# Kernel optimization log

Measured on AMD Instinct MI355X. Metric: run time of the kernel, lower is better.

Reference implementation:

```python
import jax, jax.numpy as jnp
import numpy as np

N = 50000
E = 800000
IN_F = 128
HID = 64
HEADS = 4
OUT_F = 2
NEG_SLOPE = 0.2


def setup_inputs() -> dict:
    key = jax.random.key(0)
    ks = jax.random.split(key, 16)
    feat = jax.random.normal(ks[0], (N, IN_F), dtype=jnp.float32)
    src = jax.random.randint(ks[1], (E,), 0, N, dtype=jnp.int32)
    dst = jax.random.randint(ks[2], (E,), 0, N, dtype=jnp.int32)
    s1 = 1.0 / np.sqrt(IN_F)
    s2 = 1.0 / np.sqrt(HID * HEADS)
    W1s = jax.random.uniform(ks[3], (IN_F, HEADS * HID), jnp.float32, -s1, s1)
    b1s = jnp.zeros((HEADS * HID,), jnp.float32)
    W1d = jax.random.uniform(ks[4], (IN_F, HEADS * HID), jnp.float32, -s1, s1)
    b1d = jnp.zeros((HEADS * HID,), jnp.float32)
    attn1 = jax.random.uniform(ks[5], (HEADS, HID), jnp.float32, -s1, s1)
    W2s = jax.random.uniform(ks[6], (HEADS * HID, OUT_F), jnp.float32, -s2, s2)
    b2s = jnp.zeros((OUT_F,), jnp.float32)
    W2d = jax.random.uniform(ks[7], (HEADS * HID, OUT_F), jnp.float32, -s2, s2)
    b2d = jnp.zeros((OUT_F,), jnp.float32)
    attn2 = jax.random.uniform(ks[8], (1, OUT_F), jnp.float32, -s2, s2)
    return {"feat": feat, "src": src, "dst": dst,
            "W1s": W1s, "b1s": b1s, "W1d": W1d, "b1d": b1d, "attn1": attn1,
            "W2s": W2s, "b2s": b2s, "W2d": W2d, "b2d": b2d, "attn2": attn2}


def gatv2_layer(x, src, dst, Ws, bs, Wd, bd, attn):
    # x: [N, F_in]; attn: [H, D]
    H, D = attn.shape
    hs = (x @ Ws + bs).reshape(-1, H, D)  # [N, H, D] source projection
    hd = (x @ Wd + bd).reshape(-1, H, D)  # [N, H, D] dest projection
    e = jax.nn.leaky_relu(hs[src] + hd[dst], NEG_SLOPE)        # [E, H, D]
    score = jnp.einsum('ehd,hd->eh', e, attn)                  # [E, H]
    # segment softmax over incoming edges of each dst node
    m = jax.ops.segment_max(score, dst, num_segments=N)        # [N, H]
    m = jnp.where(jnp.isfinite(m), m, 0.0)
    ex = jnp.exp(score - m[dst])                               # [E, H]
    denom = jax.ops.segment_sum(ex, dst, num_segments=N)       # [N, H]
    alpha = ex / jnp.where(denom[dst] > 0, denom[dst], 1.0)    # [E, H]
    out = jax.ops.segment_sum(alpha[:, :, None] * hs[src], dst, num_segments=N)
    return out  # [N, H, D]


def reference(feat, src, dst, W1s, b1s, W1d, b1d, attn1, W2s, b2s, W2d, b2d, attn2):
    h = gatv2_layer(feat, src, dst, W1s, b1s, W1d, b1d, attn1)  # [N, 4, 64]
    h = jax.nn.elu(h).reshape(h.shape[0], -1)                    # [N, 256]
    h = gatv2_layer(h, src, dst, W2s, b2s, W2d, b2d, attn2)      # [N, 1, 2]
    return h[:, 0, :]                                            # [N, 2]
```

## Files before the change

### kernel.cpp

```cpp
#include <hip/hip_runtime.h>
#include <math.h>

#define NN 50000
#define NE 800000
#define NEG 0.2f
#define NB 196

typedef __attribute__((ext_vector_type(8))) short bf16x8;
typedef __attribute__((ext_vector_type(4))) float f32x4;
typedef __attribute__((ext_vector_type(4))) _Float16 half4;

__device__ __forceinline__ unsigned short bf16_rne(float x)
{
    unsigned u = __float_as_uint(x);
    return (unsigned short)((u + 0x7FFF + ((u >> 16) & 1)) >> 16);
}
__device__ __forceinline__ float bf16_to_f(unsigned short h)
{
    return __uint_as_float(((unsigned)h) << 16);
}

__global__ __launch_bounds__(256) void cvt_feat(
    const float* __restrict__ f, unsigned short* __restrict__ hi,
    unsigned short* __restrict__ lo)
{
    const int i = blockIdx.x * 256 + threadIdx.x;
    if (i >= NN * 128 / 4) return;
    const float4 v = reinterpret_cast<const float4*>(f)[i];
    ushort4 h, l;
    h.x = bf16_rne(v.x); l.x = bf16_rne(v.x - bf16_to_f(h.x));
    h.y = bf16_rne(v.y); l.y = bf16_rne(v.y - bf16_to_f(h.y));
    h.z = bf16_rne(v.z); l.z = bf16_rne(v.z - bf16_to_f(h.z));
    h.w = bf16_rne(v.w); l.w = bf16_rne(v.w - bf16_to_f(h.w));
    reinterpret_cast<ushort4*>(hi)[i] = h;
    reinterpret_cast<ushort4*>(lo)[i] = l;
}

__global__ __launch_bounds__(256) void cvt_w(
    const float* __restrict__ Ws, const float* __restrict__ Wd,
    unsigned short* __restrict__ ShiP, unsigned short* __restrict__ SloP,
    unsigned short* __restrict__ DhiP, unsigned short* __restrict__ DloP)
{
    const int idx = blockIdx.x * 256 + threadIdx.x;
    const float* W = blockIdx.y ? Wd : Ws;
    unsigned short* oh = blockIdx.y ? DhiP : ShiP;
    unsigned short* ol = blockIdx.y ? DloP : SloP;
    const int j  = idx & 7;
    const int l  = (idx >> 3) & 63;
    const int ct = (idx >> 9) & 15;
    const int ks = idx >> 13;
    const int k   = ks * 32 + ((l >> 4) << 3) + j;
    const int col = (ct << 4) + (l & 15);
    const float x = W[(size_t)k * 256 + col];
    const unsigned short h = bf16_rne(x);
    oh[idx] = h;
    ol[idx] = bf16_rne(x - bf16_to_f(h));
}

__global__ __launch_bounds__(256) void gemm_mfma(
    const unsigned short* __restrict__ fhi, const unsigned short* __restrict__ flo,
    const unsigned short* __restrict__ WhS, const unsigned short* __restrict__ WlS,
    const float* __restrict__ bS, _Float16* __restrict__ outS,
    const unsigned short* __restrict__ WhD, const unsigned short* __restrict__ WlD,
    const float* __restrict__ bD, float* __restrict__ outD)
{
    const unsigned short* Wh = blockIdx.y ? WhD : WhS;
    const unsigned short* Wl = blockIdx.y ? WlD : WlS;
    const float* bv = blockIdx.y ? bD : bS;

    const int tid = threadIdx.x;
    const int w   = tid >> 6;
    const int l   = tid & 63;
    const int r16 = l & 15;
    const int kg  = l >> 4;
    const int row0 = blockIdx.x * 64;

    int arow = row0 + w * 16 + r16;
    if (arow >= NN) arow = NN - 1;

    f32x4 acc[16];
#pragma unroll
    for (int ct = 0; ct < 16; ++ct) acc[ct] = (f32x4){0.f, 0.f, 0.f, 0.f};

#pragma unroll
    for (int ks = 0; ks < 4; ++ks) {
        const bf16x8 ah = *reinterpret_cast<const bf16x8*>(
            &fhi[(size_t)arow * 128 + ks * 32 + kg * 8]);
        const bf16x8 al = *reinterpret_cast<const bf16x8*>(
            &flo[(size_t)arow * 128 + ks * 32 + kg * 8]);
#pragma unroll
        for (int ct = 0; ct < 16; ++ct) {
            const size_t boff = ((size_t)(ks * 16 + ct) * 64 + l) * 8;
            const bf16x8 bh = *reinterpret_cast<const bf16x8*>(&Wh[boff]);
            const bf16x8 bl = *reinterpret_cast<const bf16x8*>(&Wl[boff]);
            acc[ct] = __builtin_amdgcn_mfma_f32_16x16x32_bf16(ah, bh, acc[ct], 0, 0, 0);
            acc[ct] = __builtin_amdgcn_mfma_f32_16x16x32_bf16(ah, bl, acc[ct], 0, 0, 0);
            acc[ct] = __builtin_amdgcn_mfma_f32_16x16x32_bf16(al, bh, acc[ct], 0, 0, 0);
        }
    }

    const int orow0 = row0 + w * 16 + kg * 4;
    if (blockIdx.y == 0) {
#pragma unroll
        for (int ct = 0; ct < 16; ++ct) {
            const int col = ct * 16 + r16;
            const float bias = bv[col];
#pragma unroll
            for (int reg = 0; reg < 4; ++reg) {
                const int orow = orow0 + reg;
                if (orow < NN)
                    outS[(size_t)orow * 256 + col] = (_Float16)(acc[ct][reg] + bias);
            }
        }
    } else {
#pragma unroll
        for (int ct = 0; ct < 16; ++ct) {
            const int col = ct * 16 + r16;
            const float bias = bv[col];
#pragma unroll
            for (int reg = 0; reg < 4; ++reg) {
                const int orow = orow0 + reg;
                if (orow < NN)
                    outD[(size_t)orow * 256 + col] = acc[ct][reg] + bias;
            }
        }
    }
}

__global__ void count_deg(const int* __restrict__ dst, int* __restrict__ deg)
{
    int e = blockIdx.x * blockDim.x + threadIdx.x;
    if (e < NE) atomicAdd(&deg[dst[e]], 1);
}

__global__ __launch_bounds__(256) void deg_blocksum(const int* __restrict__ deg,
                                                    int* __restrict__ bsum)
{
    int i = blockIdx.x * 256 + threadIdx.x;
    int v = (i < NN) ? deg[i] : 0;
#pragma unroll
    for (int off = 32; off; off >>= 1) v += __shfl_xor(v, off);
    __shared__ int ws[4];
    if ((threadIdx.x & 63) == 0) ws[threadIdx.x >> 6] = v;
    __syncthreads();
    if (threadIdx.x == 0) bsum[blockIdx.x] = ws[0] + ws[1] + ws[2] + ws[3];
}

__global__ __launch_bounds__(256) void scan_bsum(int* __restrict__ bsum)
{
    __shared__ int tmp[256];
    int t = threadIdx.x;
    int orig = (t < NB) ? bsum[t] : 0;
    tmp[t] = orig;
    __syncthreads();
    for (int off = 1; off < 256; off <<= 1) {
        int v = (t >= off) ? tmp[t - off] : 0;
        __syncthreads();
        tmp[t] += v;
        __syncthreads();
    }
    if (t < NB) bsum[t] = tmp[t] - orig;
}

__global__ __launch_bounds__(256) void write_rows(const int* __restrict__ deg,
                                                  const int* __restrict__ bpre,
                                                  int* __restrict__ row_start,
                                                  int* __restrict__ cursor)
{
    int i = blockIdx.x * 256 + threadIdx.x;
    int d = (i < NN) ? deg[i] : 0;
    int lane = threadIdx.x & 63, w = threadIdx.x >> 6;
    int x = d;
#pragma unroll
    for (int off = 1; off < 64; off <<= 1) {
        int v = __shfl_up(x, off);
        if (lane >= off) x += v;
    }
    __shared__ int wsum[4];
    if (lane == 63) wsum[w] = x;
    __syncthreads();
    int woff = 0;
#pragma unroll
    for (int k = 0; k < 4; ++k)
        if (k < w) woff += wsum[k];
    if (i < NN) {
        int rs = bpre[blockIdx.x] + woff + x - d;
        row_start[i] = rs;
        cursor[i] = rs;
    }
    if (blockIdx.x == 0 && threadIdx.x == 0) row_start[NN] = NE;
}

__global__ void scatter_src(const int* __restrict__ src, const int* __restrict__ dst,
                            int* __restrict__ cursor, int* __restrict__ src_sorted)
{
    int e = blockIdx.x * blockDim.x + threadIdx.x;
    if (e < NE) {
        int pos = atomicAdd(&cursor[dst[e]], 1);
        src_sorted[pos] = src[e];
    }
}

__global__ __launch_bounds__(256) void gat1_fused(
    const _Float16* __restrict__ hs, const float* __restrict__ hd,
    const float* __restrict__ attn, const int* __restrict__ src_sorted,
    const int* __restrict__ row_start,
    const float* __restrict__ W2s, const float* __restrict__ b2s,
    const float* __restrict__ W2d, const float* __restrict__ b2d,
    float* __restrict__ hs2, float* __restrict__ hd2)
{
    const int n = blockIdx.x * 4 + (threadIdx.x >> 6);
    const int lane = threadIdx.x & 63;
    const int beg = row_start[n], end_ = row_start[n + 1];

    const float4 a4 = *reinterpret_cast<const float4*>(&attn[lane * 4]);
    const float4 y4 = *reinterpret_cast<const float4*>(&hd[(size_t)n * 256 + lane * 4]);

    float m = -INFINITY, den = 0.0f;
    float4 acc = make_float4(0.f, 0.f, 0.f, 0.f);

#define SCORE(xf, p)                                                        \
    {                                                                       \
        float t;                                                            \
        t = xf.x + y4.x; t = fmaxf(t, NEG * t); p = t * a4.x;               \
        t = xf.y + y4.y; t = fmaxf(t, NEG * t); p = fmaf(t, a4.y, p);       \
        t = xf.z + y4.z; t = fmaxf(t, NEG * t); p = fmaf(t, a4.z, p);       \
        t = xf.w + y4.w; t = fmaxf(t, NEG * t); p = fmaf(t, a4.w, p);       \
    }
#define UPDATE(xf, p)                                                       \
    {                                                                       \
        if (p > m + 8.0f) {                                                 \
            const float rs = __expf(m - p);                                 \
            den *= rs;                                                      \
            acc.x *= rs; acc.y *= rs; acc.z *= rs; acc.w *= rs;             \
            m = p;                                                          \
        }                                                                   \
        const float wv = __expf(p - m);                                     \
        den += wv;                                                          \
        acc.x = fmaf(wv, xf.x, acc.x);                                      \
        acc.y = fmaf(wv, xf.y, acc.y);                                      \
        acc.z = fmaf(wv, xf.z, acc.z);                                      \
        acc.w = fmaf(wv, xf.w, acc.w);                                      \
    }

    int i = beg;
    for (; i + 3 < end_; i += 4) {
        const int s0 = __builtin_amdgcn_readfirstlane(src_sorted[i]);
        const int s1 = __builtin_amdgcn_readfirstlane(src_sorted[i + 1]);
        const int s2 = __builtin_amdgcn_readfirstlane(src_sorted[i + 2]);
        const int s3 = __builtin_amdgcn_readfirstlane(src_sorted[i + 3]);
        const half4 h0 = *reinterpret_cast<const half4*>(&hs[(size_t)s0 * 256 + lane * 4]);
        const half4 h1 = *reinterpret_cast<const half4*>(&hs[(size_t)s1 * 256 + lane * 4]);
        const half4 h2 = *reinterpret_cast<const half4*>(&hs[(size_t)s2 * 256 + lane * 4]);
        const half4 h3 = *reinterpret_cast<const half4*>(&hs[(size_t)s3 * 256 + lane * 4]);
        const float4 x0 = make_float4(h0.x, h0.y, h0.z, h0.w);
        const float4 x1 = make_float4(h1.x, h1.y, h1.z, h1.w);
        const float4 x2 = make_float4(h2.x, h2.y, h2.z, h2.w);
        const float4 x3 = make_float4(h3.x, h3.y, h3.z, h3.w);
        float p0, p1, p2, p3;
        SCORE(x0, p0) SCORE(x1, p1) SCORE(x2, p2) SCORE(x3, p3)
        p0 += __shfl_xor(p0, 1); p1 += __shfl_xor(p1, 1);
        p2 += __shfl_xor(p2, 1); p3 += __shfl_xor(p3, 1);
        p0 += __shfl_xor(p0, 2); p1 += __shfl_xor(p1, 2);
        p2 += __shfl_xor(p2, 2); p3 += __shfl_xor(p3, 2);
        p0 += __shfl_xor(p0, 4); p1 += __shfl_xor(p1, 4);
        p2 += __shfl_xor(p2, 4); p3 += __shfl_xor(p3, 4);
        p0 += __shfl_xor(p0, 8); p1 += __shfl_xor(p1, 8);
        p2 += __shfl_xor(p2, 8); p3 += __shfl_xor(p3, 8);
        UPDATE(x0, p0) UPDATE(x1, p1) UPDATE(x2, p2) UPDATE(x3, p3)
    }
    for (; i < end_; ++i) {
        const int s = __builtin_amdgcn_readfirstlane(src_sorted[i]);
        const half4 hx = *reinterpret_cast<const half4*>(&hs[(size_t)s * 256 + lane * 4]);
        const float4 x = make_float4(hx.x, hx.y, hx.z, hx.w);
        float p;
        SCORE(x, p)
        p += __shfl_xor(p, 1);
        p += __shfl_xor(p, 2);
        p += __shfl_xor(p, 4);
        p += __shfl_xor(p, 8);
        UPDATE(x, p)
    }
#undef SCORE
#undef UPDATE

    const float inv = (den > 0.0f) ? 1.0f / den : 0.0f;
    float4 o;
    o.x = acc.x * inv; o.y = acc.y * inv; o.z = acc.z * inv; o.w = acc.w * inv;
    o.x = (o.x > 0.0f) ? o.x : __expf(o.x) - 1.0f;
    o.y = (o.y > 0.0f) ? o.y : __expf(o.y) - 1.0f;
    o.z = (o.z > 0.0f) ? o.z : __expf(o.z) - 1.0f;
    o.w = (o.w > 0.0f) ? o.w : __expf(o.w) - 1.0f;

    const float4 wsa = *reinterpret_cast<const float4*>(&W2s[lane * 8]);
    const float4 wsb = *reinterpret_cast<const float4*>(&W2s[lane * 8 + 4]);
    const float4 wda = *reinterpret_cast<const float4*>(&W2d[lane * 8]);
    const float4 wdb = *reinterpret_cast<const float4*>(&W2d[lane * 8 + 4]);
    float ps0 = o.x * wsa.x + o.y * wsa.z + o.z * wsb.x + o.w * wsb.z;
    float ps1 = o.x * wsa.y + o.y * wsa.w + o.z * wsb.y + o.w * wsb.w;
    float pd0 = o.x * wda.x + o.y * wda.z + o.z * wdb.x + o.w * wdb.z;
    float pd1 = o.x * wda.y + o.y * wda.w + o.z * wdb.y + o.w * wdb.w;
#pragma unroll
    for (int off = 32; off; off >>= 1) {
        ps0 += __shfl_xor(ps0, off);
        ps1 += __shfl_xor(ps1, off);
        pd0 += __shfl_xor(pd0, off);
        pd1 += __shfl_xor(pd1, off);
    }
    if (lane == 0) {
        hs2[(size_t)n * 2 + 0] = ps0 + b2s[0];
        hs2[(size_t)n * 2 + 1] = ps1 + b2s[1];
        hd2[(size_t)n * 2 + 0] = pd0 + b2d[0];
        hd2[(size_t)n * 2 + 1] = pd1 + b2d[1];
    }
}

__global__ __launch_bounds__(256) void node2_kernel(
    const float* __restrict__ hs2, const float* __restrict__ hd2,
    const float* __restrict__ attn2, const int* __restrict__ src_sorted,
    const int* __restrict__ row_start, float* __restrict__ out)
{
    const int n = blockIdx.x * 16 + (threadIdx.x >> 4);
    const int q = threadIdx.x & 15;
    if (n >= NN) return;
    const float a0 = attn2[0], a1 = attn2[1];
    const float h0 = hd2[n * 2 + 0], h1v = hd2[n * 2 + 1];
    const int beg = row_start[n], end_ = row_start[n + 1];
    float m = -INFINITY, den = 0.0f, A0 = 0.0f, A1 = 0.0f;
    for (int i = beg + q; i < end_; i += 16) {
        const int s = src_sorted[i];
        float x0 = hs2[s * 2 + 0], x1 = hs2[s * 2 + 1];
        float t0 = x0 + h0;  t0 = fmaxf(t0, NEG * t0);
        float t1 = x1 + h1v; t1 = fmaxf(t1, NEG * t1);
        float p = fmaf(t0, a0, t1 * a1);
        float mn = fmaxf(m, p);
        float c = __expf(m - mn);
        float w = __expf(p - mn);
        den = den * c + w;
        A0 = A0 * c + w * x0;
        A1 = A1 * c + w * x1;
        m = mn;
    }
#pragma unroll
    for (int off = 1; off < 16; off <<= 1) {
        float m2 = __shfl_xor(m, off, 16);
        float d2 = __shfl_xor(den, off, 16);
        float b0 = __shfl_xor(A0, off, 16);
        float b1 = __shfl_xor(A1, off, 16);
        float mn = fmaxf(m, m2);
        float c1 = (m < mn) ? __expf(m - mn) : 1.0f;
        float c2 = (m2 < mn) ? __expf(m2 - mn) : 1.0f;
        den = den * c1 + d2 * c2;
        A0 = A0 * c1 + b0 * c2;
        A1 = A1 * c1 + b1 * c2;
        m = mn;
    }
    if (q == 0) {
        out[n * 2 + 0] = (den > 0.0f) ? A0 / den : 0.0f;
        out[n * 2 + 1] = (den > 0.0f) ? A1 / den : 0.0f;
    }
}

extern "C" void kernel_launch(void* const* d_in, const int* in_sizes, int n_in,
                              void* d_out, int out_size, void* d_ws, size_t ws_size,
                              hipStream_t stream)
{
    const float* feat  = (const float*)d_in[0];
    const int*   src   = (const int*)d_in[1];
    const int*   dst   = (const int*)d_in[2];
    const float* W1s   = (const float*)d_in[3];
    const float* b1s   = (const float*)d_in[4];
    const float* W1d   = (const float*)d_in[5];
    const float* b1d   = (const float*)d_in[6];
    const float* attn1 = (const float*)d_in[7];
    const float* W2s   = (const float*)d_in[8];
    const float* b2s   = (const float*)d_in[9];
    const float* W2d   = (const float*)d_in[10];
    const float* b2d   = (const float*)d_in[11];
    const float* attn2 = (const float*)d_in[12];
    float* out = (float*)d_out;

    char* ws = (char*)d_ws;
    size_t off = 0;
    auto alloc = [&](size_t bytes) {
        char* p = ws + off;
        off += (bytes + 255) & ~size_t(255);
        return p;
    };
    _Float16*       hs1h       = (_Float16*)alloc((size_t)NN * 256 * 2);
    float*          hd1        = (float*)alloc((size_t)NN * 256 * 4);
    unsigned short* fb_hi      = (unsigned short*)alloc((size_t)NN * 128 * 2);
    unsigned short* fb_lo      = (unsigned short*)alloc((size_t)NN * 128 * 2);
    unsigned short* wbs_hi     = (unsigned short*)alloc((size_t)128 * 256 * 2);
    unsigned short* wbs_lo     = (unsigned short*)alloc((size_t)128 * 256 * 2);
    unsigned short* wbd_hi     = (unsigned short*)alloc((size_t)128 * 256 * 2);
    unsigned short* wbd_lo     = (unsigned short*)alloc((size_t)128 * 256 * 2);
    int*            src_sorted = (int*)alloc((size_t)NE * 4);
    int*            row_start  = (int*)alloc((size_t)(NN + 1) * 4);
    int*            deg        = (int*)alloc((size_t)NN * 4);
    int*            cursor     = (int*)alloc((size_t)NN * 4);
    int*            bsum       = (int*)alloc((size_t)NB * 4);
    float*          hs2        = (float*)alloc((size_t)NN * 2 * 4);
    float*          hd2        = (float*)alloc((size_t)NN * 2 * 4);
    (void)ws_size; (void)n_in; (void)in_sizes; (void)out_size;

    hipMemsetAsync(deg, 0, (size_t)NN * 4, stream);

    cvt_feat<<<(NN * 128 / 4 + 255) / 256, 256, 0, stream>>>(feat, fb_hi, fb_lo);
    dim3 wgrid(128, 2);
    cvt_w<<<wgrid, 256, 0, stream>>>(W1s, W1d, wbs_hi, wbs_lo, wbd_hi, wbd_lo);
    dim3 ggrid((NN + 63) / 64, 2);
    gemm_mfma<<<ggrid, 256, 0, stream>>>(fb_hi, fb_lo,
                                         wbs_hi, wbs_lo, b1s, hs1h,
                                         wbd_hi, wbd_lo, b1d, hd1);

    const int eb = (NE + 255) / 256;
    count_deg<<<eb, 256, 0, stream>>>(dst, deg);
    deg_blocksum<<<NB, 256, 0, stream>>>(deg, bsum);
    scan_bsum<<<1, 256, 0, stream>>>(bsum);
    write_rows<<<NB, 256, 0, stream>>>(deg, bsum, row_start, cursor);
    scatter_src<<<eb, 256, 0, stream>>>(src, dst, cursor, src_sorted);

    gat1_fused<<<NN / 4, 256, 0, stream>>>(hs1h, hd1, attn1, src_sorted, row_start,
                                           W2s, b2s, W2d, b2d, hs2, hd2);

    node2_kernel<<<(NN + 15) / 16, 256, 0, stream>>>(hs2, hd2, attn2, src_sorted,
                                                     row_start, out);
}
```

Before: 269.5 us.

## Fuse feature bf16 split into GEMM and halve-wave edge processing with fp16 dot

Removes the separate cvt_feat kernel and its hi/lo buffers by splitting fp32 features into bf16 hi/lo inside the GEMM's A-operand load. Rewrites the layer-1 aggregation so each half-wave handles a different edge, with 8 fp16 elements per lane. The leaky-relu score is computed in packed fp16 with fdot2, and the two halves' online-softmax states are merged at the end. This cuts global traffic and the instruction count per edge, at the cost of reduced score precision from fp16 arithmetic and duplicated feature conversion across the two GEMM y-blocks.

```diff
diff --git a/kernel.cpp b/kernel.cpp
--- a/kernel.cpp
+++ b/kernel.cpp
@@ -8,7 +8,10 @@
 
 typedef __attribute__((ext_vector_type(8))) short bf16x8;
 typedef __attribute__((ext_vector_type(4))) float f32x4;
-typedef __attribute__((ext_vector_type(4))) _Float16 half4;
+typedef __attribute__((ext_vector_type(8))) _Float16 half8;
+typedef __attribute__((ext_vector_type(2))) _Float16 half2v;
+
+#define PAIR(v, k) (__builtin_shufflevector(v, v, 2 * (k), 2 * (k) + 1))
 
 __device__ __forceinline__ unsigned short bf16_rne(float x)
 {
@@ -18,22 +21,6 @@
 __device__ __forceinline__ float bf16_to_f(unsigned short h)
 {
     return __uint_as_float(((unsigned)h) << 16);
-}
-
-__global__ __launch_bounds__(256) void cvt_feat(
-    const float* __restrict__ f, unsigned short* __restrict__ hi,
-    unsigned short* __restrict__ lo)
-{
-    const int i = blockIdx.x * 256 + threadIdx.x;
-    if (i >= NN * 128 / 4) return;
-    const float4 v = reinterpret_cast<const float4*>(f)[i];
-    ushort4 h, l;
-    h.x = bf16_rne(v.x); l.x = bf16_rne(v.x - bf16_to_f(h.x));
-    h.y = bf16_rne(v.y); l.y = bf16_rne(v.y - bf16_to_f(h.y));
-    h.z = bf16_rne(v.z); l.z = bf16_rne(v.z - bf16_to_f(h.z));
-    h.w = bf16_rne(v.w); l.w = bf16_rne(v.w - bf16_to_f(h.w));
-    reinterpret_cast<ushort4*>(hi)[i] = h;
-    reinterpret_cast<ushort4*>(lo)[i] = l;
 }
 
 __global__ __launch_bounds__(256) void cvt_w(
@@ -58,7 +45,7 @@
 }
 
 __global__ __launch_bounds__(256) void gemm_mfma(
-    const unsigned short* __restrict__ fhi, const unsigned short* __restrict__ flo,
+    const float* __restrict__ feat,
     const unsigned short* __restrict__ WhS, const unsigned short* __restrict__ WlS,
     const float* __restrict__ bS, _Float16* __restrict__ outS,
     const unsigned short* __restrict__ WhD, const unsigned short* __restrict__ WlD,
@@ -84,10 +71,18 @@
 
 #pragma unroll
     for (int ks = 0; ks < 4; ++ks) {
-        const bf16x8 ah = *reinterpret_cast<const bf16x8*>(
-            &fhi[(size_t)arow * 128 + ks * 32 + kg * 8]);
-        const bf16x8 al = *reinterpret_cast<const bf16x8*>(
-            &flo[(size_t)arow * 128 + ks * 32 + kg * 8]);
+        const float4 fa = *reinterpret_cast<const float4*>(
+            &feat[(size_t)arow * 128 + ks * 32 + kg * 8]);
+        const float4 fb = *reinterpret_cast<const float4*>(
+            &feat[(size_t)arow * 128 + ks * 32 + kg * 8 + 4]);
+        const float fv[8] = {fa.x, fa.y, fa.z, fa.w, fb.x, fb.y, fb.z, fb.w};
+        bf16x8 ah, al;
+#pragma unroll
+        for (int j = 0; j < 8; ++j) {
+            const unsigned short h = bf16_rne(fv[j]);
+            ah[j] = (short)h;
+            al[j] = (short)bf16_rne(fv[j] - bf16_to_f(h));
+        }
 #pragma unroll
         for (int ct = 0; ct < 16; ++ct) {
             const size_t boff = ((size_t)(ks * 16 + ct) * 64 + l) * 8;
@@ -211,107 +206,140 @@
 {
     const int n = blockIdx.x * 4 + (threadIdx.x >> 6);
     const int lane = threadIdx.x & 63;
+    const int half_id = lane >> 5;
+    const int sl = lane & 31;
     const int beg = row_start[n], end_ = row_start[n + 1];
 
-    const float4 a4 = *reinterpret_cast<const float4*>(&attn[lane * 4]);
-    const float4 y4 = *reinterpret_cast<const float4*>(&hd[(size_t)n * 256 + lane * 4]);
+    const float4 af0 = *reinterpret_cast<const float4*>(&attn[sl * 8 + 0]);
+    const float4 af1 = *reinterpret_cast<const float4*>(&attn[sl * 8 + 4]);
+    const float4 yf0 = *reinterpret_cast<const float4*>(&hd[(size_t)n * 256 + sl * 8 + 0]);
+    const float4 yf1 = *reinterpret_cast<const float4*>(&hd[(size_t)n * 256 + sl * 8 + 4]);
+    half8 ah, yh;
+    ah[0] = (_Float16)af0.x; ah[1] = (_Float16)af0.y; ah[2] = (_Float16)af0.z; ah[3] = (_Float16)af0.w;
+    ah[4] = (_Float16)af1.x; ah[5] = (_Float16)af1.y; ah[6] = (_Float16)af1.z; ah[7] = (_Float16)af1.w;
+    yh[0] = (_Float16)yf0.x; yh[1] = (_Float16)yf0.y; yh[2] = (_Float16)yf0.z; yh[3] = (_Float16)yf0.w;
+    yh[4] = (_Float16)yf1.x; yh[5] = (_Float16)yf1.y; yh[6] = (_Float16)yf1.z; yh[7] = (_Float16)yf1.w;
+    const _Float16 NEGH = (_Float16)NEG;
 
     float m = -INFINITY, den = 0.0f;
-    float4 acc = make_float4(0.f, 0.f, 0.f, 0.f);
-
-#define SCORE(xf, p)                                                        \
-    {                                                                       \
-        float t;                                                            \
-        t = xf.x + y4.x; t = fmaxf(t, NEG * t); p = t * a4.x;               \
-        t = xf.y + y4.y; t = fmaxf(t, NEG * t); p = fmaf(t, a4.y, p);       \
-        t = xf.z + y4.z; t = fmaxf(t, NEG * t); p = fmaf(t, a4.z, p);       \
-        t = xf.w + y4.w; t = fmaxf(t, NEG * t); p = fmaf(t, a4.w, p);       \
-    }
-#define UPDATE(xf, p)                                                       \
-    {                                                                       \
-        if (p > m + 8.0f) {                                                 \
-            const float rs = __expf(m - p);                                 \
-            den *= rs;                                                      \
-            acc.x *= rs; acc.y *= rs; acc.z *= rs; acc.w *= rs;             \
-            m = p;                                                          \
-        }                                                                   \
-        const float wv = __expf(p - m);                                     \
-        den += wv;                                                          \
-        acc.x = fmaf(wv, xf.x, acc.x);                                      \
-        acc.y = fmaf(wv, xf.y, acc.y);                                      \
-        acc.z = fmaf(wv, xf.z, acc.z);                                      \
-        acc.w = fmaf(wv, xf.w, acc.w);                                      \
-    }
-
-    int i = beg;
-    for (; i + 3 < end_; i += 4) {
-        const int s0 = __builtin_amdgcn_readfirstlane(src_sorted[i]);
-        const int s1 = __builtin_amdgcn_readfirstlane(src_sorted[i + 1]);
-        const int s2 = __builtin_amdgcn_readfirstlane(src_sorted[i + 2]);
-        const int s3 = __builtin_amdgcn_readfirstlane(src_sorted[i + 3]);
-        const half4 h0 = *reinterpret_cast<const half4*>(&hs[(size_t)s0 * 256 + lane * 4]);
-        const half4 h1 = *reinterpret_cast<const half4*>(&hs[(size_t)s1 * 256 + lane * 4]);
-        const half4 h2 = *reinterpret_cast<const half4*>(&hs[(size_t)s2 * 256 + lane * 4]);
-        const half4 h3 = *reinterpret_cast<const half4*>(&hs[(size_t)s3 * 256 + lane * 4]);
-        const float4 x0 = make_float4(h0.x, h0.y, h0.z, h0.w);
-        const float4 x1 = make_float4(h1.x, h1.y, h1.z, h1.w);
-        const float4 x2 = make_float4(h2.x, h2.y, h2.z, h2.w);
-        const float4 x3 = make_float4(h3.x, h3.y, h3.z, h3.w);
-        float p0, p1, p2, p3;
-        SCORE(x0, p0) SCORE(x1, p1) SCORE(x2, p2) SCORE(x3, p3)
-        p0 += __shfl_xor(p0, 1); p1 += __shfl_xor(p1, 1);
-        p2 += __shfl_xor(p2, 1); p3 += __shfl_xor(p3, 1);
-        p0 += __shfl_xor(p0, 2); p1 += __shfl_xor(p1, 2);
-        p2 += __shfl_xor(p2, 2); p3 += __shfl_xor(p3, 2);
-        p0 += __shfl_xor(p0, 4); p1 += __shfl_xor(p1, 4);
-        p2 += __shfl_xor(p2, 4); p3 += __shfl_xor(p3, 4);
-        p0 += __shfl_xor(p0, 8); p1 += __shfl_xor(p1, 8);
-        p2 += __shfl_xor(p2, 8); p3 += __shfl_xor(p3, 8);
-        UPDATE(x0, p0) UPDATE(x1, p1) UPDATE(x2, p2) UPDATE(x3, p3)
-    }
-    for (; i < end_; ++i) {
-        const int s = __builtin_amdgcn_readfirstlane(src_sorted[i]);
-        const half4 hx = *reinterpret_cast<const half4*>(&hs[(size_t)s * 256 + lane * 4]);
-        const float4 x = make_float4(hx.x, hx.y, hx.z, hx.w);
+    float acc[8];
+#pragma unroll
+    for (int j = 0; j < 8; ++j) acc[j] = 0.0f;
+
+#define SCORE(xh, p)                                                         \
+    {                                                                        \
+        half8 t = xh + yh;                                                   \
+        half8 tn = t * NEGH;                                                 \
+        t = __builtin_elementwise_max(t, tn);                                \
+        p = __builtin_amdgcn_fdot2(PAIR(t, 0), PAIR(ah, 0), 0.0f, false);    \
+        p = __builtin_amdgcn_fdot2(PAIR(t, 1), PAIR(ah, 1), p, false);       \
+        p = __builtin_amdgcn_fdot2(PAIR(t, 2), PAIR(ah, 2), p, false);       \
+        p = __builtin_amdgcn_fdot2(PAIR(t, 3), PAIR(ah, 3), p, false);       \
+    }
+#define UPDATE(xh, wv)                                                       \
+    {                                                                        \
+        den += wv;                                                           \
+        _Pragma("unroll")                                                    \
+        for (int j = 0; j < 8; ++j)                                          \
+            acc[j] = fmaf(wv, (float)xh[j], acc[j]);                         \
+    }
+#define RESCALE(p)                                                           \
+    if (p > m + 8.0f) {                                                      \
+        const float rs = __expf(m - p);                                      \
+        den *= rs;                                                           \
+        _Pragma("unroll")                                                    \
+        for (int j = 0; j < 8; ++j) acc[j] *= rs;                            \
+        m = p;                                                               \
+    }
+
+    int base = beg;
+    for (; base + 3 < end_; base += 4) {
+        const int sA = src_sorted[base + half_id];
+        const int sB = src_sorted[base + 2 + half_id];
+        const half8 xA = *reinterpret_cast<const half8*>(&hs[(size_t)sA * 256 + sl * 8]);
+        const half8 xB = *reinterpret_cast<const half8*>(&hs[(size_t)sB * 256 + sl * 8]);
+        float pA, pB;
+        SCORE(xA, pA)
+        SCORE(xB, pB)
+        pA += __shfl_xor(pA, 1);  pB += __shfl_xor(pB, 1);
+        pA += __shfl_xor(pA, 2);  pB += __shfl_xor(pB, 2);
+        pA += __shfl_xor(pA, 4);  pB += __shfl_xor(pB, 4);
+        RESCALE(pA)
+        const float wA = __expf(pA - m);
+        UPDATE(xA, wA)
+        RESCALE(pB)
+        const float wB = __expf(pB - m);
+        UPDATE(xB, wB)
+    }
+    for (; base < end_; base += 2) {
+        const int ei = base + half_id;
+        const bool valid = ei < end_;
+        const int eic = valid ? ei : end_ - 1;
+        const int s = src_sorted[eic];
+        const half8 x = *reinterpret_cast<const half8*>(&hs[(size_t)s * 256 + sl * 8]);
         float p;
         SCORE(x, p)
         p += __shfl_xor(p, 1);
         p += __shfl_xor(p, 2);
         p += __shfl_xor(p, 4);
-        p += __shfl_xor(p, 8);
-        UPDATE(x, p)
+        if (!valid) p = -INFINITY;
+        RESCALE(p)
+        const float wv = valid ? __expf(p - m) : 0.0f;
+        UPDATE(x, wv)
     }
 #undef SCORE
 #undef UPDATE
+#undef RESCALE
+
+    {
+        const float mo = __shfl_xor(m, 32);
+        const float dno = __shfl_xor(den, 32);
+        const float M = fmaxf(m, mo);
+        const float s1 = (m > -INFINITY) ? __expf(m - M) : 0.0f;
+        const float s2 = (mo > -INFINITY) ? __expf(mo - M) : 0.0f;
+        den = den * s1 + dno * s2;
+#pragma unroll
+        for (int j = 0; j < 8; ++j) {
+            const float av = __shfl_xor(acc[j], 32);
+            acc[j] = acc[j] * s1 + av * s2;
+        }
+    }
 
     const float inv = (den > 0.0f) ? 1.0f / den : 0.0f;
-    float4 o;
-    o.x = acc.x * inv; o.y = acc.y * inv; o.z = acc.z * inv; o.w = acc.w * inv;
-    o.x = (o.x > 0.0f) ? o.x : __expf(o.x) - 1.0f;
-    o.y = (o.y > 0.0f) ? o.y : __expf(o.y) - 1.0f;
-    o.z = (o.z > 0.0f) ? o.z : __expf(o.z) - 1.0f;
-    o.w = (o.w > 0.0f) ? o.w : __expf(o.w) - 1.0f;
-
-    const float4 wsa = *reinterpret_cast<const float4*>(&W2s[lane * 8]);
-    const float4 wsb = *reinterpret_cast<const float4*>(&W2s[lane * 8 + 4]);
-    const float4 wda = *reinterpret_cast<const float4*>(&W2d[lane * 8]);
-    const float4 wdb = *reinterpret_cast<const float4*>(&W2d[lane * 8 + 4]);
-    float ps0 = o.x * wsa.x + o.y * wsa.z + o.z * wsb.x + o.w * wsb.z;
-    float ps1 = o.x * wsa.y + o.y * wsa.w + o.z * wsb.y + o.w * wsb.w;
-    float pd0 = o.x * wda.x + o.y * wda.z + o.z * wdb.x + o.w * wdb.z;
-    float pd1 = o.x * wda.y + o.y * wda.w + o.z * wdb.y + o.w * wdb.w;
-#pragma unroll
-    for (int off = 32; off; off >>= 1) {
+    float o[8];
+#pragma unroll
+    for (int j = 0; j < 8; ++j) {
+        float v = acc[j] * inv;
+        o[j] = (v > 0.0f) ? v : __expf(v) - 1.0f;
+    }
+    const float4 wsA = *reinterpret_cast<const float4*>(&W2s[sl * 16 + 0]);
+    const float4 wsB = *reinterpret_cast<const float4*>(&W2s[sl * 16 + 4]);
+    const float4 wsC = *reinterpret_cast<const float4*>(&W2s[sl * 16 + 8]);
+    const float4 wsD = *reinterpret_cast<const float4*>(&W2s[sl * 16 + 12]);
+    const float4 wdA = *reinterpret_cast<const float4*>(&W2d[sl * 16 + 0]);
+    const float4 wdB = *reinterpret_cast<const float4*>(&W2d[sl * 16 + 4]);
+    const float4 wdC = *reinterpret_cast<const float4*>(&W2d[sl * 16 + 8]);
+    const float4 wdD = *reinterpret_cast<const float4*>(&W2d[sl * 16 + 12]);
+    float ps0 = o[0] * wsA.x + o[1] * wsA.z + o[2] * wsB.x + o[3] * wsB.z
+              + o[4] * wsC.x + o[5] * wsC.z + o[6] * wsD.x + o[7] * wsD.z;
+    float ps1 = o[0] * wsA.y + o[1] * wsA.w + o[2] * wsB.y + o[3] * wsB.w
+              + o[4] * wsC.y + o[5] * wsC.w + o[6] * wsD.y + o[7] * wsD.w;
+    float pd0 = o[0] * wdA.x + o[1] * wdA.z + o[2] * wdB.x + o[3] * wdB.z
+              + o[4] * wdC.x + o[5] * wdC.z + o[6] * wdD.x + o[7] * wdD.z;
+    float pd1 = o[0] * wdA.y + o[1] * wdA.w + o[2] * wdB.y + o[3] * wdB.w
+              + o[4] * wdC.y + o[5] * wdC.w + o[6] * wdD.y + o[7] * wdD.w;
+#pragma unroll
+    for (int off = 1; off < 64; off <<= 1) {
         ps0 += __shfl_xor(ps0, off);
         ps1 += __shfl_xor(ps1, off);
         pd0 += __shfl_xor(pd0, off);
         pd1 += __shfl_xor(pd1, off);
     }
     if (lane == 0) {
-        hs2[(size_t)n * 2 + 0] = ps0 + b2s[0];
-        hs2[(size_t)n * 2 + 1] = ps1 + b2s[1];
-        hd2[(size_t)n * 2 + 0] = pd0 + b2d[0];
-        hd2[(size_t)n * 2 + 1] = pd1 + b2d[1];
+        hs2[(size_t)n * 2 + 0] = ps0 * 0.5f + b2s[0];
+        hs2[(size_t)n * 2 + 1] = ps1 * 0.5f + b2s[1];
+        hd2[(size_t)n * 2 + 0] = pd0 * 0.5f + b2d[0];
+        hd2[(size_t)n * 2 + 1] = pd1 * 0.5f + b2d[1];
     }
 }
 
@@ -389,8 +417,6 @@
     };
     _Float16*       hs1h       = (_Float16*)alloc((size_t)NN * 256 * 2);
     float*          hd1        = (float*)alloc((size_t)NN * 256 * 4);
-    unsigned short* fb_hi      = (unsigned short*)alloc((size_t)NN * 128 * 2);
-    unsigned short* fb_lo      = (unsigned short*)alloc((size_t)NN * 128 * 2);
     unsigned short* wbs_hi     = (unsigned short*)alloc((size_t)128 * 256 * 2);
     unsigned short* wbs_lo     = (unsigned short*)alloc((size_t)128 * 256 * 2);
     unsigned short* wbd_hi     = (unsigned short*)alloc((size_t)128 * 256 * 2);
@@ -406,11 +432,10 @@
 
     hipMemsetAsync(deg, 0, (size_t)NN * 4, stream);
 
-    cvt_feat<<<(NN * 128 / 4 + 255) / 256, 256, 0, stream>>>(feat, fb_hi, fb_lo);
     dim3 wgrid(128, 2);
     cvt_w<<<wgrid, 256, 0, stream>>>(W1s, W1d, wbs_hi, wbs_lo, wbd_hi, wbd_lo);
     dim3 ggrid((NN + 63) / 64, 2);
-    gemm_mfma<<<ggrid, 256, 0, stream>>>(fb_hi, fb_lo,
+    gemm_mfma<<<ggrid, 256, 0, stream>>>(feat,
                                          wbs_hi, wbs_lo, b1s, hs1h,
                                          wbd_hi, wbd_lo, b1d, hd1);
 
```

Result: slower. 276.9 us (+2.8%).
